# Kernel tuning notes

Hardware: AMD Instinct MI355X
Metric: run time of the kernel (lower is better)

The kernel has to match this reference:

```python
import jax, jax.numpy as jnp
import numpy as np

B, Q, HID = 16, 1, 1024
LH, LD = 32, 128            # large num heads / large head dim
BLOCK, NBPS = 16, 64        # cache block size, blocks per sequence
NBLK, MAXLEN = B * NBPS, NBPS * BLOCK
ROPE_BASE = 10000.0


def setup_inputs() -> dict:
    key = jax.random.key(0)
    ks = jax.random.split(key, 6)
    hidden_states = jax.random.normal(ks[0], (B, Q, HID), jnp.float32)
    q_proj_w = jax.random.normal(ks[1], (LH * LD, HID), jnp.float32) * 0.02
    o_proj_w = jax.random.normal(ks[2], (HID, LH * LD), jnp.float32) * 0.02
    k_cache = jax.random.normal(ks[3], (NBLK, LH, BLOCK, LD), jnp.float32)
    v_cache = jax.random.normal(ks[4], (NBLK, LH, BLOCK, LD), jnp.float32)
    # each sequence owns NBPS distinct cache blocks
    block_tables = jnp.arange(NBLK, dtype=jnp.int32).reshape(B, NBPS)
    sequence_lengths = jax.random.randint(ks[5], (B,), 1, MAXLEN + 1).astype(jnp.int32)
    position_ids = (sequence_lengths - 1).astype(jnp.int32).reshape(B, Q)
    return dict(hidden_states=hidden_states, q_proj_w=q_proj_w, o_proj_w=o_proj_w,
                k_cache=k_cache, v_cache=v_cache, block_tables=block_tables,
                sequence_lengths=sequence_lengths, position_ids=position_ids,
                n_spec_tokens=5)


def _rotate_half(x):
    h = x.shape[-1] // 2
    return jnp.concatenate([-x[..., h:], x[..., :h]], axis=-1)


def reference(hidden_states, q_proj_w, o_proj_w, k_cache, v_cache,
              block_tables, sequence_lengths, position_ids, n_spec_tokens):
    # q projection -> [B, Q, LH, LD]
    q = (hidden_states @ q_proj_w.T).reshape(B, Q, LH, LD)
    # RoPE at positions shifted by n_spec_tokens
    pos = (position_ids + n_spec_tokens).astype(jnp.float32)              # [B, Q]
    inv_freq = 1.0 / (ROPE_BASE ** (jnp.arange(0, LD, 2, dtype=jnp.float32) / LD))
    freqs = pos[..., None] * inv_freq                                      # [B, Q, LD/2]
    emb = jnp.concatenate([freqs, freqs], axis=-1)                         # [B, Q, LD]
    cos = jnp.cos(emb)[:, :, None, :]
    sin = jnp.sin(emb)[:, :, None, :]
    q = q * cos + _rotate_half(q) * sin
    q = q.reshape(B * Q, LH, LD)  # q_len == 1 -> [B, LH, LD]
    # gather paged KV: [B, NBPS, LH, BLOCK, LD] -> [B, L, LH, LD]
    k = k_cache[block_tables].transpose(0, 1, 3, 2, 4).reshape(B, MAXLEN, LH, LD)
    v = v_cache[block_tables].transpose(0, 1, 3, 2, 4).reshape(B, MAXLEN, LH, LD)
    scale = float(1.0 / np.sqrt(LD))
    scores = jnp.einsum('bhd,blhd->bhl', q, k) * scale                     # [B, LH, L]
    valid = jnp.arange(MAXLEN)[None, :] < sequence_lengths[:, None]        # [B, L]
    scores = jnp.where(valid[:, None, :], scores, -jnp.inf)
    attn = jax.nn.softmax(scores, axis=-1)
    out = jnp.einsum('bhl,blhd->bhd', attn, v).reshape(B, Q, LH * LD)
    return out @ o_proj_w.T                                                # [B, Q, HID]
```

## Files before the change

kernel.cpp:

```cpp
#include <hip/hip_runtime.h>
#include <hip/hip_bf16.h>
#include <math.h>

#define B_   16
#define HID_ 1024
#define LH_  32
#define LD_  128
#define BLOCK_ 16
#define NBPS_  64
#define MAXLEN_ 1024
#define SPLIT_ 16
#define CHUNK_ (MAXLEN_ / SPLIT_)

typedef float vf4 __attribute__((ext_vector_type(4)));

__global__ __launch_bounds__(256) void qproj_rope_kernel(const float* __restrict__ hs,
                                                         const float* __restrict__ w,
                                                         const int* __restrict__ pid,
                                                         const int* __restrict__ nsp,
                                                         float* __restrict__ q) {
    int t = threadIdx.x;
    int h = blockIdx.x >> 4;
    int g = blockIdx.x & 15;
    int j = t >> 6;
    int lane = t & 63;
    int d = g * 4 + j;
    int r0 = h * 128 + d;
    int r1 = r0 + 64;

    vf4 w0[4], w1[4];
#pragma unroll
    for (int s = 0; s < 4; ++s) {
        w0[s] = *(const vf4*)&w[(size_t)r0 * HID_ + s * 256 + lane * 4];
        w1[s] = *(const vf4*)&w[(size_t)r1 * HID_ + s * 256 + lane * 4];
    }

    __shared__ float ssum[8][16];
    for (int b = 0; b < B_; ++b) {
        float p0 = 0.f, p1 = 0.f;
#pragma unroll
        for (int s = 0; s < 4; ++s) {
            vf4 a = *(const vf4*)&hs[b * 1024 + s * 256 + lane * 4];
            p0 += w0[s].x*a.x + w0[s].y*a.y + w0[s].z*a.z + w0[s].w*a.w;
            p1 += w1[s].x*a.x + w1[s].y*a.y + w1[s].z*a.z + w1[s].w*a.w;
        }
#pragma unroll
        for (int o = 1; o < 64; o <<= 1) { p0 += __shfl_xor(p0, o); p1 += __shfl_xor(p1, o); }
        if (lane == 0) { ssum[j][b] = p0; ssum[j + 4][b] = p1; }
    }
    __syncthreads();
    if (t < 64) {
        int jj = t >> 4;
        int b  = t & 15;
        int dd = g * 4 + jj;
        double x0 = (double)ssum[jj][b];
        double x1 = (double)ssum[jj + 4][b];
        double pos = (double)(pid[b] + nsp[0]);
        double inv_freq = 1.0 / pow(10000.0, (double)dd * (1.0 / 64.0));
        double f = pos * inv_freq;
        double cs = cos(f), sn = sin(f);
        const double scale = 0.08838834764831845;
        int base = b * 4096 + h * LD_ + dd;
        q[base]      = (float)((x0 * cs - x1 * sn) * scale);
        q[base + 64] = (float)((x1 * cs + x0 * sn) * scale);
    }
}

__global__ __launch_bounds__(256) void attn_kernel(const float* __restrict__ q,
                                                   const float* __restrict__ kc,
                                                   const float* __restrict__ vc,
                                                   const int* __restrict__ btab,
                                                   const int* __restrict__ slen,
                                                   float* __restrict__ pml,
                                                   float* __restrict__ pacc) {
    int c = blockIdx.x, h = blockIdx.y, b = blockIdx.z;
    int L = slen[b];
    int start = c * CHUNK_;
    if (start >= L) return;

    int bh = b * LH_ + h;
    int pbase = bh * SPLIT_ + c;
    int t = threadIdx.x;
    int lane = t & 63, wv = t >> 6;
    int sg = lane >> 4;
    int lg = lane & 15;
    int d0 = lg * 8;
    int po = wv * 4 + sg;
    const float* qp = q + (size_t)bh * LD_ + d0;
    vf4 qa = *(const vf4*)qp;
    vf4 qb = *(const vf4*)(qp + 4);

    int end = min(start + CHUNK_, L);
    int blkr[4];
#pragma unroll
    for (int i = 0; i < 4; ++i) blkr[i] = btab[b * NBPS_ + c * 4 + i];

    float m = -INFINITY, l = 0.f;
    float acc[8];
#pragma unroll
    for (int k = 0; k < 8; ++k) acc[k] = 0.f;

    int i = 0;
#pragma unroll 4
    for (int pos = start + po; pos < end; pos += 16, ++i) {
        size_t off = (((size_t)blkr[i] * LH_ + h) * BLOCK_ + po) * LD_ + d0;
        vf4 k0 = *(const vf4*)(kc + off);
        vf4 k1 = *(const vf4*)(kc + off + 4);
        vf4 v0 = *(const vf4*)(vc + off);
        vf4 v1 = *(const vf4*)(vc + off + 4);

        float dot = qa.x*k0.x + qa.y*k0.y + qa.z*k0.z + qa.w*k0.w
                  + qb.x*k1.x + qb.y*k1.y + qb.z*k1.z + qb.w*k1.w;
#pragma unroll
        for (int o = 1; o < 16; o <<= 1) dot += __shfl_xor(dot, o);

        float mn = fmaxf(m, dot);
        float r = (m >= mn) ? 1.f : __expf(m - mn);
        float p = __expf(dot - mn);
        l = l * r + p;
        acc[0] = acc[0]*r + p*v0.x;  acc[1] = acc[1]*r + p*v0.y;
        acc[2] = acc[2]*r + p*v0.z;  acc[3] = acc[3]*r + p*v0.w;
        acc[4] = acc[4]*r + p*v1.x;  acc[5] = acc[5]*r + p*v1.y;
        acc[6] = acc[6]*r + p*v1.z;  acc[7] = acc[7]*r + p*v1.w;
        m = mn;
    }

#pragma unroll
    for (int o = 16; o < 64; o <<= 1) {
        float m2 = __shfl_xor(m, o), l2 = __shfl_xor(l, o);
        float a2[8];
#pragma unroll
        for (int k = 0; k < 8; ++k) a2[k] = __shfl_xor(acc[k], o);
        float mn = fmaxf(m, m2);
        float ra = (m  >= mn) ? 1.f : __expf(m  - mn);
        float rb = (m2 >= mn) ? 1.f : __expf(m2 - mn);
        l = l * ra + l2 * rb;
#pragma unroll
        for (int k = 0; k < 8; ++k) acc[k] = acc[k]*ra + a2[k]*rb;
        m = mn;
    }

    __shared__ float sm[4], sl_[4], sacc[4][128];
    if (lane < 16) {
#pragma unroll
        for (int k = 0; k < 8; ++k) sacc[wv][d0 + k] = acc[k];
        if (lane == 0) { sm[wv] = m; sl_[wv] = l; }
    }
    __syncthreads();

    if (t < 64) {
        float M = fmaxf(fmaxf(sm[0], sm[1]), fmaxf(sm[2], sm[3]));
        int d = t * 2;
        float lt = 0.f, o0 = 0.f, o1 = 0.f;
#pragma unroll
        for (int w2 = 0; w2 < 4; ++w2) {
            float mw = sm[w2];
            float e = (mw >= M) ? 1.f : __expf(mw - M);
            lt += e * sl_[w2];
            o0 += e * sacc[w2][d];
            o1 += e * sacc[w2][d + 1];
        }
        pacc[(size_t)pbase * 128 + d]     = o0;
        pacc[(size_t)pbase * 128 + d + 1] = o1;
        if (t == 0) { pml[pbase * 2] = M; pml[pbase * 2 + 1] = lt; }
    }
}

__global__ __launch_bounds__(64) void combine_kernel(const float* __restrict__ pml,
                                                     const float* __restrict__ pacc,
                                                     const int* __restrict__ slen,
                                                     float* __restrict__ attn) {
    int bh = blockIdx.x;
    int b = bh >> 5;
    int cmax = (slen[b] + CHUNK_ - 1) >> 6;
    int lane = threadIdx.x;
    float M = -INFINITY;
    for (int c = 0; c < cmax; ++c) M = fmaxf(M, pml[(bh * SPLIT_ + c) * 2]);
    int d = lane * 2;
    float lt = 0.f, o0 = 0.f, o1 = 0.f;
    for (int c = 0; c < cmax; ++c) {
        float mc = pml[(bh * SPLIT_ + c) * 2];
        float e = (mc >= M) ? 1.f : __expf(mc - M);
        lt += e * pml[(bh * SPLIT_ + c) * 2 + 1];
        o0 += e * pacc[((size_t)bh * SPLIT_ + c) * 128 + d];
        o1 += e * pacc[((size_t)bh * SPLIT_ + c) * 128 + d + 1];
    }
    float inv = 1.f / lt;
    attn[(size_t)bh * LD_ + d]     = o0 * inv;
    attn[(size_t)bh * LD_ + d + 1] = o1 * inv;
}

__global__ __launch_bounds__(256) void oproj_kernel(const float* __restrict__ attn,
                                                    const float* __restrict__ w,
                                                    float* __restrict__ out) {
    int t = threadIdx.x;
    int row0 = blockIdx.x * 2;
    int lane = t & 63, wv = t >> 6;

    vf4 wr0[4], wr1[4];
#pragma unroll
    for (int s = 0; s < 4; ++s) {
        wr0[s] = *(const vf4*)&w[(size_t)row0 * 4096 + s * 1024 + t * 4];
        wr1[s] = *(const vf4*)&w[(size_t)(row0 + 1) * 4096 + s * 1024 + t * 4];
    }

    __shared__ float lds[2][4][16];
    for (int b = 0; b < B_; ++b) {
        float p0 = 0.f, p1 = 0.f;
#pragma unroll
        for (int s = 0; s < 4; ++s) {
            vf4 a = *(const vf4*)&attn[b * 4096 + s * 1024 + t * 4];
            p0 += wr0[s].x*a.x + wr0[s].y*a.y + wr0[s].z*a.z + wr0[s].w*a.w;
            p1 += wr1[s].x*a.x + wr1[s].y*a.y + wr1[s].z*a.z + wr1[s].w*a.w;
        }
#pragma unroll
        for (int o = 1; o < 64; o <<= 1) { p0 += __shfl_xor(p0, o); p1 += __shfl_xor(p1, o); }
        if (lane == 0) { lds[0][wv][b] = p0; lds[1][wv][b] = p1; }
    }
    __syncthreads();
    if (t < 32) {
        int r = t >> 4, b = t & 15;
        out[b * HID_ + row0 + r] =
            lds[r][0][b] + lds[r][1][b] + lds[r][2][b] + lds[r][3][b];
    }
}

extern "C" void kernel_launch(void* const* d_in, const int* in_sizes, int n_in,
                              void* d_out, int out_size, void* d_ws, size_t ws_size,
                              hipStream_t stream) {
    const float* hs   = (const float*)d_in[0];
    const float* qw   = (const float*)d_in[1];
    const float* ow   = (const float*)d_in[2];
    const float* kc   = (const float*)d_in[3];
    const float* vc   = (const float*)d_in[4];
    const int*   btab = (const int*)d_in[5];
    const int*   slen = (const int*)d_in[6];
    const int*   pid  = (const int*)d_in[7];
    const int*   nsp  = (const int*)d_in[8];
    float* out = (float*)d_out;
    float* ws  = (float*)d_ws;

    float* q_ws    = ws;
    float* attn_ws = ws + 65536;
    float* pml     = ws + 131072;
    float* pacc    = ws + 147456;

    qproj_rope_kernel<<<512, 256, 0, stream>>>(hs, qw, pid, nsp, q_ws);
    attn_kernel<<<dim3(SPLIT_, LH_, B_), 256, 0, stream>>>(q_ws, kc, vc, btab, slen, pml, pacc);
    combine_kernel<<<B_ * LH_, 64, 0, stream>>>(pml, pacc, slen, attn_ws);
    oproj_kernel<<<512, 256, 0, stream>>>(attn_ws, ow, out);
}
```

Baseline: 110.4 us.

## Give each wavefront its own cache block split and drop in-block LDS merge

```diff
diff --git a/kernel.cpp b/kernel.cpp
--- a/kernel.cpp
+++ b/kernel.cpp
@@ -9,7 +9,7 @@
 #define BLOCK_ 16
 #define NBPS_  64
 #define MAXLEN_ 1024
-#define SPLIT_ 16
+#define SPLIT_ 64
 #define CHUNK_ (MAXLEN_ / SPLIT_)
 
 typedef float vf4 __attribute__((ext_vector_type(4)));
@@ -73,37 +73,36 @@
                                                    const int* __restrict__ slen,
                                                    float* __restrict__ pml,
                                                    float* __restrict__ pacc) {
-    int c = blockIdx.x, h = blockIdx.y, b = blockIdx.z;
+    int t = threadIdx.x;
+    int wv = t >> 6, lane = t & 63;
+    int c = blockIdx.x * 4 + wv;
+    int h = blockIdx.y, b = blockIdx.z;
     int L = slen[b];
     int start = c * CHUNK_;
     if (start >= L) return;
 
     int bh = b * LH_ + h;
     int pbase = bh * SPLIT_ + c;
-    int t = threadIdx.x;
-    int lane = t & 63, wv = t >> 6;
     int sg = lane >> 4;
     int lg = lane & 15;
     int d0 = lg * 8;
-    int po = wv * 4 + sg;
+
     const float* qp = q + (size_t)bh * LD_ + d0;
     vf4 qa = *(const vf4*)qp;
     vf4 qb = *(const vf4*)(qp + 4);
 
-    int end = min(start + CHUNK_, L);
-    int blkr[4];
-#pragma unroll
-    for (int i = 0; i < 4; ++i) blkr[i] = btab[b * NBPS_ + c * 4 + i];
+    int nv = min(CHUNK_, L - start);
+    int blk = btab[b * NBPS_ + c];
+    size_t base = (((size_t)blk * LH_ + h) * BLOCK_) * LD_ + d0;
 
     float m = -INFINITY, l = 0.f;
     float acc[8];
 #pragma unroll
     for (int k = 0; k < 8; ++k) acc[k] = 0.f;
 
-    int i = 0;
 #pragma unroll 4
-    for (int pos = start + po; pos < end; pos += 16, ++i) {
-        size_t off = (((size_t)blkr[i] * LH_ + h) * BLOCK_ + po) * LD_ + d0;
+    for (int p = sg; p < nv; p += 4) {
+        size_t off = base + (size_t)p * LD_;
         vf4 k0 = *(const vf4*)(kc + off);
         vf4 k1 = *(const vf4*)(kc + off + 4);
         vf4 v0 = *(const vf4*)(vc + off);
@@ -116,12 +115,12 @@
 
         float mn = fmaxf(m, dot);
         float r = (m >= mn) ? 1.f : __expf(m - mn);
-        float p = __expf(dot - mn);
-        l = l * r + p;
-        acc[0] = acc[0]*r + p*v0.x;  acc[1] = acc[1]*r + p*v0.y;
-        acc[2] = acc[2]*r + p*v0.z;  acc[3] = acc[3]*r + p*v0.w;
-        acc[4] = acc[4]*r + p*v1.x;  acc[5] = acc[5]*r + p*v1.y;
-        acc[6] = acc[6]*r + p*v1.z;  acc[7] = acc[7]*r + p*v1.w;
+        float p2 = __expf(dot - mn);
+        l = l * r + p2;
+        acc[0] = acc[0]*r + p2*v0.x;  acc[1] = acc[1]*r + p2*v0.y;
+        acc[2] = acc[2]*r + p2*v0.z;  acc[3] = acc[3]*r + p2*v0.w;
+        acc[4] = acc[4]*r + p2*v1.x;  acc[5] = acc[5]*r + p2*v1.y;
+        acc[6] = acc[6]*r + p2*v1.z;  acc[7] = acc[7]*r + p2*v1.w;
         m = mn;
     }
 
@@ -140,29 +139,13 @@
         m = mn;
     }
 
-    __shared__ float sm[4], sl_[4], sacc[4][128];
     if (lane < 16) {
-#pragma unroll
-        for (int k = 0; k < 8; ++k) sacc[wv][d0 + k] = acc[k];
-        if (lane == 0) { sm[wv] = m; sl_[wv] = l; }
-    }
-    __syncthreads();
-
-    if (t < 64) {
-        float M = fmaxf(fmaxf(sm[0], sm[1]), fmaxf(sm[2], sm[3]));
-        int d = t * 2;
-        float lt = 0.f, o0 = 0.f, o1 = 0.f;
-#pragma unroll
-        for (int w2 = 0; w2 < 4; ++w2) {
-            float mw = sm[w2];
-            float e = (mw >= M) ? 1.f : __expf(mw - M);
-            lt += e * sl_[w2];
-            o0 += e * sacc[w2][d];
-            o1 += e * sacc[w2][d + 1];
-        }
-        pacc[(size_t)pbase * 128 + d]     = o0;
-        pacc[(size_t)pbase * 128 + d + 1] = o1;
-        if (t == 0) { pml[pbase * 2] = M; pml[pbase * 2 + 1] = lt; }
+        float* pd = pacc + (size_t)pbase * 128 + d0;
+        vf4 s0 = {acc[0], acc[1], acc[2], acc[3]};
+        vf4 s1 = {acc[4], acc[5], acc[6], acc[7]};
+        *(vf4*)pd = s0;
+        *(vf4*)(pd + 4) = s1;
+        if (lane == 0) { pml[pbase * 2] = m; pml[pbase * 2 + 1] = l; }
     }
 }
 
@@ -172,7 +155,7 @@
                                                      float* __restrict__ attn) {
     int bh = blockIdx.x;
     int b = bh >> 5;
-    int cmax = (slen[b] + CHUNK_ - 1) >> 6;
+    int cmax = (slen[b] + CHUNK_ - 1) >> 4;
     int lane = threadIdx.x;
     float M = -INFINITY;
     for (int c = 0; c < cmax; ++c) M = fmaxf(M, pml[(bh * SPLIT_ + c) * 2]);
@@ -243,10 +226,10 @@
     float* q_ws    = ws;
     float* attn_ws = ws + 65536;
     float* pml     = ws + 131072;
-    float* pacc    = ws + 147456;
+    float* pacc    = ws + 196608;
 
     qproj_rope_kernel<<<512, 256, 0, stream>>>(hs, qw, pid, nsp, q_ws);
-    attn_kernel<<<dim3(SPLIT_, LH_, B_), 256, 0, stream>>>(q_ws, kc, vc, btab, slen, pml, pacc);
+    attn_kernel<<<dim3(SPLIT_ / 4, LH_, B_), 256, 0, stream>>>(q_ws, kc, vc, btab, slen, pml, pacc);
     combine_kernel<<<B_ * LH_, 64, 0, stream>>>(pml, pacc, slen, attn_ws);
     oproj_kernel<<<512, 256, 0, stream>>>(attn_ws, ow, out);
 }
```

Result: slower. 128.6 us (+16.5%).
